# Kernel tuning notes

Measured on AMD Instinct MI355X. Metric: run time of the kernel, lower is better.

Reference implementation:

```python
import jax, jax.numpy as jnp
import numpy as np

B, NJ, NM = 64, 30, 20
N = NJ * NM          # 600 operation nodes per FJSP instance
IN_DIM, H = 2, 128


def _bn(h):
    # torch BatchNorm1d in training mode, gamma=1/beta=0 (module init), stats over all nodes
    m = h.mean(axis=(0, 1))
    v = h.var(axis=(0, 1))
    return (h - m) / jnp.sqrt(v + 1e-5)


def setup_inputs() -> dict:
    key = jax.random.key(0)
    ks = jax.random.split(key, 20)
    x = jax.random.normal(ks[0], (B, N, IN_DIM), jnp.float32)
    graph_pool = jnp.full((B, N), 1.0 / N, jnp.float32)   # average graph pooling weights
    padded_nei = jnp.zeros((1,), jnp.int32)               # unused (sum pooling path)
    adj = (jax.random.uniform(ks[1], (B, N, N)) < 0.01).astype(jnp.float32)
    adj = jnp.minimum(adj + jnp.eye(N, dtype=jnp.float32)[None], 1.0)  # self-loops
    candidate = jax.random.randint(ks[2], (B, NJ), 0, N)
    a_index = jax.random.randint(ks[3], (B,), 0, NJ)
    mask = jax.random.uniform(ks[4], (B, NJ)) < 0.2
    mask = mask.at[jnp.arange(B), a_index].set(False)     # chosen action never masked
    mask_mch = jax.random.uniform(ks[5], (B, N, NM)) < 0.3
    dur = jax.random.uniform(ks[6], (B, N, NM), dtype=jnp.float32)
    old_action = jax.random.randint(ks[7], (B,), 0, N)
    mch_pool = jax.random.normal(ks[8], (B, H), jnp.float32)

    def w(k, i, o):
        return jax.random.normal(k, (i, o), jnp.float32) * (1.0 / np.sqrt(i))

    z = lambda n: jnp.zeros((n,), jnp.float32)            # biases init to 0 in module
    return dict(
        x=x, graph_pool=graph_pool, padded_nei=padded_nei, adj=adj,
        candidate=candidate, mask=mask, mask_mch=mask_mch, dur=dur,
        a_index=a_index, old_action=old_action, mch_pool=mch_pool,
        W1_0=w(ks[9], IN_DIM, H), b1_0=z(H), W2_0=w(ks[10], H, H), b2_0=z(H),
        W1_1=w(ks[11], H, H), b1_1=z(H), W2_1=w(ks[12], H, H), b2_1=z(H),
        Wa1=w(ks[13], 3 * H, H), ba1=z(H), Wa2=w(ks[14], H, H), ba2=z(H),
        Wa3=w(ks[15], H, 1), ba3=z(1),
        Wc1=w(ks[16], H, H), bc1=z(H), Wc2=w(ks[17], H, 1), bc2=z(1),
    )


def reference(x, graph_pool, padded_nei, adj, candidate, mask, mask_mch, dur,
              a_index, old_action, mch_pool,
              W1_0, b1_0, W2_0, b2_0, W1_1, b1_1, W2_1, b2_1,
              Wa1, ba1, Wa2, ba2, Wa3, ba3, Wc1, bc1, Wc2, bc2):
    # --- GIN encoder: num_layers-1 = 2 message-passing layers, sum pooling ---
    h = x
    for (W1, b1, W2, b2) in ((W1_0, b1_0, W2_0, b2_0), (W1_1, b1_1, W2_1, b2_1)):
        pooled = jnp.einsum('bnm,bmd->bnd', adj, h)         # neighbor sum (adj has self-loops)
        h1 = jax.nn.relu(_bn(pooled @ W1 + b1))             # MLP hidden (BN inside MLP)
        h = jax.nn.relu(_bn(h1 @ W2 + b2))                  # layer BN + relu
    h_nodes = h                                             # [B, N, H]
    h_pooled = jnp.einsum('bn,bnd->bd', graph_pool, h_nodes)  # [B, H]

    # --- gather candidate features, concat pooled contexts ---
    cand_feat = jnp.take_along_axis(h_nodes, candidate[:, :, None], axis=1)  # [B, NJ, H]
    concat = jnp.concatenate([
        cand_feat,
        jnp.broadcast_to(h_pooled[:, None, :], cand_feat.shape),
        jnp.broadcast_to(mch_pool[:, None, :], cand_feat.shape)], axis=-1)   # [B, NJ, 3H]

    # --- MLPActor(3 layers, tanh) ---
    a = jnp.tanh(concat @ Wa1 + ba1)
    a = jnp.tanh(a @ Wa2 + ba2)
    scores = (a @ Wa3 + ba3).squeeze(-1) * 10.0             # [B, NJ]
    scores = jnp.where(mask, -jnp.inf, scores)
    logpi = jax.nn.log_softmax(scores, axis=1)
    pi = jnp.exp(logpi)
    log_a = jnp.take_along_axis(logpi, a_index[:, None], axis=1)[:, 0]
    entropy = -jnp.sum(jnp.where(pi > 0, pi * logpi, 0.0), axis=1)

    # --- gather action-dependent tensors (detached in torch) ---
    b_idx = jnp.arange(B)
    action_node = dur[b_idx, old_action]                    # [B, NM]
    action_feature = h_nodes[b_idx, old_action]             # [B, H]
    mask_mch_action = mask_mch[b_idx, old_action][:, None, :]  # [B, 1, NM]

    # --- MLPCritic(2 layers, tanh) ---
    v = jnp.tanh(h_pooled @ Wc1 + bc1) @ Wc2 + bc2          # [B, 1]

    sg = jax.lax.stop_gradient
    return (entropy, v, log_a, sg(action_node), sg(action_feature),
            mask_mch_action, sg(h_pooled))
```

## Files before the change

kernel.cpp:

```cpp
#include <hip/hip_runtime.h>
#include <hip/hip_bf16.h>

#define BB 64
#define NJ 30
#define NM 20
#define NN 600
#define HH 128
#define NROWS (BB*NN)
#define CAP 48

typedef __attribute__((ext_vector_type(8))) short short8;
typedef __attribute__((ext_vector_type(4))) float f32x4;

#define STATS_B   0
#define HPOOL_B   4096
#define FLAGS_B   36864
#define ZERO_B    36880
#define WTB_B     37120
#define SCORES_B  135424
#define NBRCNT_B  143104
#define NBRIDX_B  296704
#define POOLED0_B 7669504
#define T1_B      7976704
#define P1_B      27637504

#define OUT_ENT   0
#define OUT_V     64
#define OUT_LOGA  128
#define OUT_ANODE 192
#define OUT_AFEAT 1472
#define OUT_MMCH  9664
#define OUT_HPOOL 10944

__device__ __forceinline__ bool mask_at(const void* p, int layout, long i) {
    if (layout == 2) return ((const float*)p)[i] != 0.f;
    if (layout == 1) return ((const unsigned char*)p)[i] != 0;
    return ((const int*)p)[i] != 0;
}

__device__ __forceinline__ short bf16rne(float f) {
    unsigned u = __float_as_uint(f);
    return (short)((u + 0x7fffu + ((u >> 16) & 1u)) >> 16);
}
__device__ __forceinline__ float bf2f(unsigned h) {
    return __uint_as_float(h << 16);
}
__device__ __forceinline__ unsigned packbf(float a, float b) {
    return ((unsigned)(unsigned short)bf16rne(a)) |
           (((unsigned)(unsigned short)bf16rne(b)) << 16);
}

__global__ __launch_bounds__(256) void k_pre(const void* mask_p, const void* maskmch_p,
                                             int* flags,
                                             const float* __restrict__ Wa,
                                             const float* __restrict__ Wb,
                                             const float* __restrict__ Wc,
                                             unsigned short* __restrict__ wT) {
    int bid = blockIdx.x;
    int tid = threadIdx.x;
    if (bid >= 97) {
        int bid2 = bid - 97;
        int mat = bid2 >> 6;
        int idx = ((bid2 & 63) << 8) + tid;
        const float* W = mat == 0 ? Wa : (mat == 1 ? Wb : Wc);
        int k = idx >> 7, c = idx & 127;
        wT[mat * 16384 + c * HH + k] = (unsigned short)bf16rne(W[idx]);
        return;
    }
    unsigned agg = 0;
    int which;
    if (bid == 0) {
        which = 0;
        const unsigned* p = (const unsigned*)mask_p;
        unsigned w0 = (tid < 480) ? p[tid] : 0u;
        unsigned w1 = (tid + 256 < 480) ? p[tid + 256] : 0u;
        agg = w0 | w1;
    } else {
        which = 1;
        const unsigned* p = (const unsigned*)maskmch_p + (size_t)(bid - 1) * 200;
        agg = (tid < 200) ? p[tid] : 0u;
    }
    int f = 0;
    if (((agg >> 24) & 0xffu) == 0x3fu) f |= 1;
    if ((((agg >> 8) & 0xffu) == 1u) || (((agg >> 16) & 0xffu) == 1u) ||
        (((agg >> 24) & 0xffu) == 1u)) f |= 2;
#pragma unroll
    for (int off = 1; off < 64; off <<= 1) f |= __shfl_xor(f, off);
    if ((tid & 63) == 0 && f) atomicOr(&flags[which], f);
}

__global__ __launch_bounds__(256) void k_sparse(const float* __restrict__ adj,
                                                const float* __restrict__ x,
                                                int* __restrict__ nbr_cnt,
                                                int* __restrict__ nbr_idx,
                                                float* __restrict__ pooled0) {
    int wrow = blockIdx.x * 4 + (threadIdx.x >> 6);
    int lane = threadIdx.x & 63;
    int b = wrow / NN;
    const float4* arow = (const float4*)(adj + (size_t)wrow * NN);
    int* irow = nbr_idx + (size_t)wrow * CAP;
    const float* xb = x + (size_t)b * NN * 2;
    float4 vv[3];
    vv[0] = arow[lane];
    vv[1] = arow[64 + lane];
    vv[2] = (128 + lane < 150) ? arow[128 + lane] : make_float4(0.f, 0.f, 0.f, 0.f);
    int cnt = 0;
    float p0 = 0.f, p1 = 0.f;
#pragma unroll
    for (int it = 0; it < 3; ++it) {
        float4 v = vv[it];
        int col0 = it * 256 + lane * 4;
        bool m0 = v.x != 0.f, m1 = v.y != 0.f, m2 = v.z != 0.f, m3 = v.w != 0.f;
        int c_lane = (int)m0 + (int)m1 + (int)m2 + (int)m3;
        int inc = c_lane;
#pragma unroll
        for (int off = 1; off < 64; off <<= 1) {
            int t = __shfl_up(inc, off);
            if (lane >= off) inc += t;
        }
        int pos = cnt + inc - c_lane;
        if (m0) {
            if (pos < CAP) irow[pos] = col0;
            float2 xv = *(const float2*)&xb[col0 * 2];
            p0 += xv.x; p1 += xv.y; ++pos;
        }
        if (m1) {
            if (pos < CAP) irow[pos] = col0 + 1;
            float2 xv = *(const float2*)&xb[(col0 + 1) * 2];
            p0 += xv.x; p1 += xv.y; ++pos;
        }
        if (m2) {
            if (pos < CAP) irow[pos] = col0 + 2;
            float2 xv = *(const float2*)&xb[(col0 + 2) * 2];
            p0 += xv.x; p1 += xv.y; ++pos;
        }
        if (m3) {
            if (pos < CAP) irow[pos] = col0 + 3;
            float2 xv = *(const float2*)&xb[(col0 + 3) * 2];
            p0 += xv.x; p1 += xv.y; ++pos;
        }
        cnt += __shfl(inc, 63);
    }
#pragma unroll
    for (int off = 1; off < 64; off <<= 1) {
        p0 += __shfl_xor(p0, off);
        p1 += __shfl_xor(p1, off);
    }
    if (lane == 0) {
        nbr_cnt[wrow] = cnt < CAP ? cnt : CAP;
        pooled0[(size_t)wrow * 2]     = p0;
        pooled0[(size_t)wrow * 2 + 1] = p1;
    }
}

__global__ __launch_bounds__(256) void k_p0stats(const float* __restrict__ pooled0,
                                                 float* __restrict__ out5) {
    __shared__ float red[4][5];
    int i = blockIdx.x * 256 + threadIdx.x;
    float p0 = pooled0[(size_t)i * 2], p1 = pooled0[(size_t)i * 2 + 1];
    float v[5] = {p0, p1, p0 * p0, p1 * p1, p0 * p1};
#pragma unroll
    for (int j = 0; j < 5; ++j)
#pragma unroll
        for (int off = 1; off < 64; off <<= 1) v[j] += __shfl_xor(v[j], off);
    int lane = threadIdx.x & 63, w = threadIdx.x >> 6;
    if (lane == 0)
#pragma unroll
        for (int j = 0; j < 5; ++j) red[w][j] = v[j];
    __syncthreads();
    if (threadIdx.x == 0)
#pragma unroll
        for (int j = 0; j < 5; ++j)
            atomicAdd(&out5[j], red[0][j] + red[1][j] + red[2][j] + red[3][j]);
}

template<int MODE>
__global__ __launch_bounds__(256) void k_stage(const void* __restrict__ t_in_v,
                                               const float* __restrict__ pooled0,
                                               const float* __restrict__ W1,
                                               const unsigned short* __restrict__ wT,
                                               const float* __restrict__ stats_in,
                                               unsigned short* __restrict__ t_out,
                                               float* __restrict__ stats_out) {
    __shared__ float sm_mean[HH], sm_inv[HH];
    __shared__ float smS[4][32], smQ[4][32];
    int tid = threadIdx.x;
    if (MODE == 0 && tid < HH) {
        float S0 = stats_in[0], S1 = stats_in[1], Q0 = stats_in[2], Q1 = stats_in[3], P01 = stats_in[4];
        float w0 = W1[tid], w1 = W1[HH + tid];
        float m = (S0 * w0 + S1 * w1) * (1.f / NROWS);
        float eq = (Q0 * w0 * w0 + Q1 * w1 * w1 + 2.f * P01 * w0 * w1) * (1.f / NROWS);
        sm_mean[tid] = m;
        sm_inv[tid] = 1.f / sqrtf(eq - m * m + 1e-5f);
    }
    if (MODE == 1 && tid < HH) {
        float s = stats_in[tid], q = stats_in[HH + tid];
        float m = s * (1.f / NROWS);
        sm_mean[tid] = m;
        sm_inv[tid] = 1.f / sqrtf(q * (1.f / NROWS) - m * m + 1e-5f);
    }
    if (MODE != 2) __syncthreads();

    const unsigned short* tin = (const unsigned short*)t_in_v;
    int lane = tid & 63, wave = tid >> 6;
    int r16 = lane & 15, kg = lane >> 4;
    int rowbase = (blockIdx.x >> 2) * 64 + wave * 16;
    int colq = blockIdx.x & 3;

    f32x4 acc[2];
#pragma unroll
    for (int t = 0; t < 2; ++t)
#pragma unroll
        for (int i = 0; i < 4; ++i) acc[t][i] = 0.f;

    float p0 = 0.f, p1 = 0.f;
    if (MODE == 0) {
        p0 = pooled0[(size_t)(rowbase + r16) * 2];
        p1 = pooled0[(size_t)(rowbase + r16) * 2 + 1];
    }

#pragma unroll
    for (int ks = 0; ks < 4; ++ks) {
        int kb = ks * 32 + kg * 8;
        short8 afr;
        if (MODE == 2) {
            afr = *(const short8*)&tin[(size_t)(rowbase + r16) * HH + kb];
        } else {
            float av[8];
            if (MODE == 0) {
                float4 wa0 = *(const float4*)&W1[kb];
                float4 wa1 = *(const float4*)&W1[kb + 4];
                float4 wb0 = *(const float4*)&W1[HH + kb];
                float4 wb1 = *(const float4*)&W1[HH + kb + 4];
                av[0] = p0 * wa0.x + p1 * wb0.x; av[1] = p0 * wa0.y + p1 * wb0.y;
                av[2] = p0 * wa0.z + p1 * wb0.z; av[3] = p0 * wa0.w + p1 * wb0.w;
                av[4] = p0 * wa1.x + p1 * wb1.x; av[5] = p0 * wa1.y + p1 * wb1.y;
                av[6] = p0 * wa1.z + p1 * wb1.z; av[7] = p0 * wa1.w + p1 * wb1.w;
            } else {
                short8 raw = *(const short8*)&tin[(size_t)(rowbase + r16) * HH + kb];
#pragma unroll
                for (int j = 0; j < 8; ++j) av[j] = bf2f((unsigned short)raw[j]);
            }
            float4 m0 = *(const float4*)&sm_mean[kb];
            float4 m1 = *(const float4*)&sm_mean[kb + 4];
            float4 i0 = *(const float4*)&sm_inv[kb];
            float4 i1 = *(const float4*)&sm_inv[kb + 4];
            av[0] = fmaxf((av[0] - m0.x) * i0.x, 0.f);
            av[1] = fmaxf((av[1] - m0.y) * i0.y, 0.f);
            av[2] = fmaxf((av[2] - m0.z) * i0.z, 0.f);
            av[3] = fmaxf((av[3] - m0.w) * i0.w, 0.f);
            av[4] = fmaxf((av[4] - m1.x) * i1.x, 0.f);
            av[5] = fmaxf((av[5] - m1.y) * i1.y, 0.f);
            av[6] = fmaxf((av[6] - m1.z) * i1.z, 0.f);
            av[7] = fmaxf((av[7] - m1.w) * i1.w, 0.f);
#pragma unroll
            for (int j = 0; j < 8; ++j) afr[j] = bf16rne(av[j]);
        }
#pragma unroll
        for (int t = 0; t < 2; ++t) {
            short8 bfr = *(const short8*)&wT[(size_t)((colq * 2 + t) * 16 + r16) * HH + kb];
            acc[t] = __builtin_amdgcn_mfma_f32_16x16x32_bf16(afr, bfr, acc[t], 0, 0, 0);
        }
    }

#pragma unroll
    for (int t = 0; t < 2; ++t) {
        int lc = t * 16 + r16;
        int col = colq * 32 + lc;
        float s = 0.f, q = 0.f;
#pragma unroll
        for (int i = 0; i < 4; ++i) {
            float v = acc[t][i];
            t_out[(size_t)(rowbase + kg * 4 + i) * HH + col] = (unsigned short)bf16rne(v);
            s += v; q += v * v;
        }
        s += __shfl_xor(s, 16); q += __shfl_xor(q, 16);
        s += __shfl_xor(s, 32); q += __shfl_xor(q, 32);
        if (kg == 0) { smS[wave][lc] = s; smQ[wave][lc] = q; }
    }
    __syncthreads();
    if (tid < 32) {
        int col = colq * 32 + tid;
        atomicAdd(&stats_out[col],      smS[0][tid] + smS[1][tid] + smS[2][tid] + smS[3][tid]);
        atomicAdd(&stats_out[HH + col], smQ[0][tid] + smQ[1][tid] + smQ[2][tid] + smQ[3][tid]);
    }
}

__global__ __launch_bounds__(256) void k_pool1(const unsigned short* __restrict__ t1,
                                               const int* __restrict__ nbr_cnt,
                                               const int* __restrict__ nbr_idx,
                                               const float* __restrict__ stats1,
                                               unsigned short* __restrict__ pooled1) {
    __shared__ float sm_mean[HH], sm_inv[HH];
    int tid = threadIdx.x;
    if (tid < HH) {
        float s = stats1[tid], q = stats1[HH + tid];
        float m = s * (1.f / NROWS);
        sm_mean[tid] = m;
        sm_inv[tid] = 1.f / sqrtf(q * (1.f / NROWS) - m * m + 1e-5f);
    }
    __syncthreads();
    int c4 = tid & 31, rl = tid >> 5;
    int row = blockIdx.x * 8 + rl;
    int b = row / NN;
    float4 mm = *(const float4*)&sm_mean[c4 * 4];
    float4 iv = *(const float4*)&sm_inv[c4 * 4];
    int cnt = nbr_cnt[row];
    const int* ir = nbr_idx + (size_t)row * CAP;
    const unsigned short* tb = t1 + (size_t)b * NN * HH;
    float a0 = 0.f, a1 = 0.f, a2 = 0.f, a3 = 0.f;
    int i = 0;
    for (; i + 1 < cnt; i += 2) {
        int m0 = ir[i], m1 = ir[i + 1];
        uint2 w0 = *(const uint2*)&tb[(size_t)m0 * HH + c4 * 4];
        uint2 w1 = *(const uint2*)&tb[(size_t)m1 * HH + c4 * 4];
        a0 += fmaxf((bf2f(w0.x & 0xffffu) - mm.x) * iv.x, 0.f)
            + fmaxf((bf2f(w1.x & 0xffffu) - mm.x) * iv.x, 0.f);
        a1 += fmaxf((bf2f(w0.x >> 16)     - mm.y) * iv.y, 0.f)
            + fmaxf((bf2f(w1.x >> 16)     - mm.y) * iv.y, 0.f);
        a2 += fmaxf((bf2f(w0.y & 0xffffu) - mm.z) * iv.z, 0.f)
            + fmaxf((bf2f(w1.y & 0xffffu) - mm.z) * iv.z, 0.f);
        a3 += fmaxf((bf2f(w0.y >> 16)     - mm.w) * iv.w, 0.f)
            + fmaxf((bf2f(w1.y >> 16)     - mm.w) * iv.w, 0.f);
    }
    if (i < cnt) {
        int m0 = ir[i];
        uint2 w0 = *(const uint2*)&tb[(size_t)m0 * HH + c4 * 4];
        a0 += fmaxf((bf2f(w0.x & 0xffffu) - mm.x) * iv.x, 0.f);
        a1 += fmaxf((bf2f(w0.x >> 16)     - mm.y) * iv.y, 0.f);
        a2 += fmaxf((bf2f(w0.y & 0xffffu) - mm.z) * iv.z, 0.f);
        a3 += fmaxf((bf2f(w0.y >> 16)     - mm.w) * iv.w, 0.f);
    }
    uint2 o;
    o.x = packbf(a0, a1);
    o.y = packbf(a2, a3);
    *(uint2*)&pooled1[(size_t)row * HH + c4 * 4] = o;
}

__global__ __launch_bounds__(256) void k_hpool(const unsigned short* __restrict__ t3,
                                               const float* __restrict__ gp,
                                               const float* __restrict__ stats3,
                                               float* __restrict__ hpool) {
    __shared__ float sm_mean[HH], sm_inv[HH];
    __shared__ float red[8][HH];
    int tid = threadIdx.x;
    if (tid < HH) {
        float s = stats3[tid], q = stats3[HH + tid];
        float m = s * (1.f / NROWS);
        sm_mean[tid] = m;
        sm_inv[tid] = 1.f / sqrtf(q * (1.f / NROWS) - m * m + 1e-5f);
    }
    __syncthreads();
    int b = blockIdx.x >> 3, chunk = blockIdx.x & 7;
    int c4 = tid & 31, rl = tid >> 5;
    float4 mm = *(const float4*)&sm_mean[c4 * 4];
    float4 iv = *(const float4*)&sm_inv[c4 * 4];
    float a0 = 0.f, a1 = 0.f, a2 = 0.f, a3 = 0.f;
    int nend = chunk * 75 + 75;
    for (int n = chunk * 75 + rl; n < nend; n += 8) {
        float w = gp[b * NN + n];
        uint2 t = *(const uint2*)&t3[((size_t)b * NN + n) * HH + c4 * 4];
        a0 += w * fmaxf((bf2f(t.x & 0xffffu) - mm.x) * iv.x, 0.f);
        a1 += w * fmaxf((bf2f(t.x >> 16)     - mm.y) * iv.y, 0.f);
        a2 += w * fmaxf((bf2f(t.y & 0xffffu) - mm.z) * iv.z, 0.f);
        a3 += w * fmaxf((bf2f(t.y >> 16)     - mm.w) * iv.w, 0.f);
    }
    *(float4*)&red[rl][c4 * 4] = make_float4(a0, a1, a2, a3);
    __syncthreads();
    if (tid < HH) {
        float s = 0.f;
#pragma unroll
        for (int g = 0; g < 8; ++g) s += red[g][tid];
        atomicAdd(&hpool[b * HH + tid], s);
    }
}

__global__ __launch_bounds__(256) void k_actor(const unsigned short* __restrict__ t3,
                                               const int* __restrict__ cand,
                                               const float* __restrict__ hpool,
                                               const float* __restrict__ mch,
                                               const float* __restrict__ stats3,
                                               const float* __restrict__ Wa1,
                                               const float* __restrict__ ba1,
                                               const float* __restrict__ Wa2,
                                               const float* __restrict__ ba2,
                                               const float* __restrict__ Wa3,
                                               const float* __restrict__ ba3,
                                               float* __restrict__ scores) {
    __shared__ float sh_c[8 * 384];
    __shared__ float sh_a1[8 * HH];
    __shared__ float sred[8][HH];
    int tid = threadIdx.x;
    int rbase = blockIdx.x * 8;
    int c = tid & 127, slot = tid >> 7;

    float mean_c, inv_c;
    {
        float s = stats3[c], q = stats3[HH + c];
        float m = s * (1.f / NROWS);
        mean_c = m;
        inv_c = 1.f / sqrtf(q * (1.f / NROWS) - m * m + 1e-5f);
    }
#pragma unroll
    for (int rr = 0; rr < 4; ++rr) {
        int r = slot * 4 + rr;
        int row = rbase + r;
        int b = row / NJ;
        int cd = cand[row];
        float v = bf2f(t3[((size_t)b * NN + cd) * HH + c]);
        sh_c[r * 384 + c]       = fmaxf((v - mean_c) * inv_c, 0.f);
        sh_c[r * 384 + 128 + c] = hpool[b * HH + c];
        sh_c[r * 384 + 256 + c] = mch[b * HH + c];
    }
    __syncthreads();

    float acc[4] = {0.f, 0.f, 0.f, 0.f};
    for (int k = 0; k < 384; ++k) {
        float w = Wa1[(size_t)k * HH + c];
#pragma unroll
        for (int rr = 0; rr < 4; ++rr)
            acc[rr] += sh_c[(slot * 4 + rr) * 384 + k] * w;
    }
    float bb = ba1[c];
#pragma unroll
    for (int rr = 0; rr < 4; ++rr)
        sh_a1[(slot * 4 + rr) * HH + c] = tanhf(acc[rr] + bb);
    __syncthreads();

    float acc2[4] = {0.f, 0.f, 0.f, 0.f};
    for (int k = 0; k < HH; ++k) {
        float w = Wa2[(size_t)k * HH + c];
#pragma unroll
        for (int rr = 0; rr < 4; ++rr)
            acc2[rr] += sh_a1[(slot * 4 + rr) * HH + k] * w;
    }
    float w3 = Wa3[c], bb2 = ba2[c];
#pragma unroll
    for (int rr = 0; rr < 4; ++rr)
        sred[slot * 4 + rr][c] = tanhf(acc2[rr] + bb2) * w3;
    __syncthreads();
    int r = tid >> 5, l32 = tid & 31;
    float v = sred[r][l32] + sred[r][l32 + 32] + sred[r][l32 + 64] + sred[r][l32 + 96];
    v += __shfl_xor(v, 1); v += __shfl_xor(v, 2); v += __shfl_xor(v, 4);
    v += __shfl_xor(v, 8); v += __shfl_xor(v, 16);
    if (l32 == 0) scores[rbase + r] = 10.f * (v + ba3[0]);
}

__global__ __launch_bounds__(128) void k_final(const unsigned short* __restrict__ t3,
                                               const float* __restrict__ stats3,
                                               const float* __restrict__ hpool,
                                               const float* __restrict__ scores,
                                               const void* __restrict__ mask_p,
                                               const void* __restrict__ maskmch_p,
                                               const int* __restrict__ flags,
                                               const float* __restrict__ dur,
                                               const int* __restrict__ a_index,
                                               const int* __restrict__ old_action,
                                               const float* __restrict__ Wc1,
                                               const float* __restrict__ bc1,
                                               const float* __restrict__ Wc2,
                                               const float* __restrict__ bc2,
                                               float* __restrict__ out) {
    __shared__ float sm_mean[HH], sm_inv[HH], sh_hp[HH], sh_red[HH];
    __shared__ float sh_s[32], sh_lp[32];
    __shared__ int sh_m[32];
    int b = blockIdx.x, t = threadIdx.x;
    {
        float s = stats3[t], q = stats3[HH + t];
        float m = s * (1.f / NROWS);
        sm_mean[t] = m;
        sm_inv[t] = 1.f / sqrtf(q * (1.f / NROWS) - m * m + 1e-5f);
    }
    sh_hp[t] = hpool[b * HH + t];
    __syncthreads();

    float acc = bc1[t];
    for (int k = 0; k < HH; ++k) acc += sh_hp[k] * Wc1[k * HH + t];
    sh_red[t] = tanhf(acc) * Wc2[t];
    __syncthreads();
    for (int st = 64; st > 0; st >>= 1) {
        if (t < st) sh_red[t] += sh_red[t + st];
        __syncthreads();
    }
    if (t == 0) out[OUT_V + b] = sh_red[0] + bc2[0];

    int fA = flags[0], fB = flags[1];
    int layA = (fA & 1) ? 2 : ((fA & 2) ? 1 : 0);
    int layB = (fB & 1) ? 2 : ((fB & 2) ? 1 : 0);
    if (t < NJ) {
        sh_s[t] = scores[b * NJ + t];
        sh_m[t] = mask_at(mask_p, layA, (long)b * NJ + t) ? 1 : 0;
    }
    __syncthreads();
    if (t == 0) {
        float mx = -1e30f;
        for (int j = 0; j < NJ; ++j)
            if (!sh_m[j] && sh_s[j] > mx) mx = sh_s[j];
        float sum = 0.f;
        for (int j = 0; j < NJ; ++j)
            if (!sh_m[j]) sum += expf(sh_s[j] - mx);
        float lse = mx + logf(sum);
        float ent = 0.f;
        for (int j = 0; j < NJ; ++j) {
            if (!sh_m[j]) {
                float lp = sh_s[j] - lse;
                sh_lp[j] = lp;
                float pi = expf(lp);
                if (pi > 0.f) ent -= pi * lp;
            }
        }
        out[OUT_ENT + b] = ent;
        out[OUT_LOGA + b] = sh_lp[a_index[b]];
    }

    int old = old_action[b];
    if (t < NM) {
        out[OUT_ANODE + b * NM + t] = dur[((size_t)b * NN + old) * NM + t];
        out[OUT_MMCH + b * NM + t] =
            mask_at(maskmch_p, layB, ((size_t)b * NN + old) * NM + t) ? 1.f : 0.f;
    }
    {
        float v = bf2f(t3[((size_t)b * NN + old) * HH + t]);
        out[OUT_AFEAT + b * HH + t] = fmaxf((v - sm_mean[t]) * sm_inv[t], 0.f);
        out[OUT_HPOOL + b * HH + t] = sh_hp[t];
    }
}

extern "C" void kernel_launch(void* const* d_in, const int* in_sizes, int n_in,
                              void* d_out, int out_size, void* d_ws, size_t ws_size,
                              hipStream_t stream) {
    (void)in_sizes; (void)n_in; (void)out_size; (void)ws_size;
    const float* x         = (const float*)d_in[0];
    const float* gp        = (const float*)d_in[1];
    const float* adj       = (const float*)d_in[3];
    const int*   cand      = (const int*)d_in[4];
    const void*  mask_p    = d_in[5];
    const void*  maskmch_p = d_in[6];
    const float* dur       = (const float*)d_in[7];
    const int*   a_index   = (const int*)d_in[8];
    const int*   old_act   = (const int*)d_in[9];
    const float* mch_pool  = (const float*)d_in[10];
    const float* W1_0 = (const float*)d_in[11];
    const float* W2_0 = (const float*)d_in[13];
    const float* W1_1 = (const float*)d_in[15];
    const float* W2_1 = (const float*)d_in[17];
    const float* Wa1  = (const float*)d_in[19];
    const float* ba1  = (const float*)d_in[20];
    const float* Wa2  = (const float*)d_in[21];
    const float* ba2  = (const float*)d_in[22];
    const float* Wa3  = (const float*)d_in[23];
    const float* ba3  = (const float*)d_in[24];
    const float* Wc1  = (const float*)d_in[25];
    const float* bc1  = (const float*)d_in[26];
    const float* Wc2  = (const float*)d_in[27];
    const float* bc2  = (const float*)d_in[28];

    char* ws = (char*)d_ws;
    float* stats   = (float*)(ws + STATS_B);
    float* hpool   = (float*)(ws + HPOOL_B);
    int*   flags   = (int*)(ws + FLAGS_B);
    unsigned short* wtb = (unsigned short*)(ws + WTB_B);
    float* scores  = (float*)(ws + SCORES_B);
    int*   nbr_cnt = (int*)(ws + NBRCNT_B);
    int*   nbr_idx = (int*)(ws + NBRIDX_B);
    float* pooled0 = (float*)(ws + POOLED0_B);
    unsigned short* t1_16 = (unsigned short*)(ws + T1_B);
    unsigned short* p1_16 = (unsigned short*)(ws + P1_B);
    float* out     = (float*)d_out;

    hipMemsetAsync(ws, 0, ZERO_B, stream);
    k_pre<<<289, 256, 0, stream>>>(mask_p, maskmch_p, flags, W2_0, W1_1, W2_1, wtb);
    k_sparse<<<NROWS / 4, 256, 0, stream>>>(adj, x, nbr_cnt, nbr_idx, pooled0);
    k_p0stats<<<NROWS / 256, 256, 0, stream>>>(pooled0, stats);
    k_stage<0><<<2400, 256, 0, stream>>>(nullptr, pooled0, W1_0, wtb, stats, t1_16, stats + 256);
    k_pool1<<<NROWS / 8, 256, 0, stream>>>(t1_16, nbr_cnt, nbr_idx, stats + 256, p1_16);
    k_stage<2><<<2400, 256, 0, stream>>>(p1_16, nullptr, nullptr, wtb + 16384, stats, t1_16, stats + 512);
    k_stage<1><<<2400, 256, 0, stream>>>(t1_16, nullptr, nullptr, wtb + 32768, stats + 512, p1_16, stats + 768);
    k_hpool<<<BB * 8, 256, 0, stream>>>(p1_16, gp, stats + 768, hpool);
    k_actor<<<240, 256, 0, stream>>>(p1_16, cand, hpool, mch_pool, stats + 768,
                                     Wa1, ba1, Wa2, ba2, Wa3, ba3, scores);
    k_final<<<BB, 128, 0, stream>>>(p1_16, stats + 768, hpool, scores, mask_p, maskmch_p, flags,
                                    dur, a_index, old_act, Wc1, bc1, Wc2, bc2, out);
}
```

Measured before the change: 352.1 us.

## Fuse preprocessing into sparse pass, pooling into GEMM stage, and tail kernels

Folds the mask-flag and weight-transpose work into the sparse adjacency kernel. Fuses the layer-1 neighbour pooling with the following MFMA GEMM through shared memory, so the pooled intermediate is never written to global memory. Merges graph pooling, the actor MLP, the critic and the final softmax into one per-batch kernel, with the hpool/mch part of the first actor layer computed once per batch. This cuts the launch count from ten to six and removes several global round trips, but the tail now runs on only 64 blocks, and the pooling GEMM reads weights from global memory per block.

After: 395.7 us. 12.4% more time.

```diff
diff --git a/kernel.cpp b/kernel.cpp
--- a/kernel.cpp
+++ b/kernel.cpp
@@ -13,11 +13,9 @@
 typedef __attribute__((ext_vector_type(4))) float f32x4;
 
 #define STATS_B   0
-#define HPOOL_B   4096
 #define FLAGS_B   36864
 #define ZERO_B    36880
 #define WTB_B     37120
-#define SCORES_B  135424
 #define NBRCNT_B  143104
 #define NBRIDX_B  296704
 #define POOLED0_B 7669504
@@ -50,52 +48,53 @@
            (((unsigned)(unsigned short)bf16rne(b)) << 16);
 }
 
-__global__ __launch_bounds__(256) void k_pre(const void* mask_p, const void* maskmch_p,
-                                             int* flags,
-                                             const float* __restrict__ Wa,
-                                             const float* __restrict__ Wb,
-                                             const float* __restrict__ Wc,
-                                             unsigned short* __restrict__ wT) {
-    int bid = blockIdx.x;
-    int tid = threadIdx.x;
-    if (bid >= 97) {
-        int bid2 = bid - 97;
-        int mat = bid2 >> 6;
-        int idx = ((bid2 & 63) << 8) + tid;
-        const float* W = mat == 0 ? Wa : (mat == 1 ? Wb : Wc);
-        int k = idx >> 7, c = idx & 127;
-        wT[mat * 16384 + c * HH + k] = (unsigned short)bf16rne(W[idx]);
-        return;
-    }
-    unsigned agg = 0;
-    int which;
-    if (bid == 0) {
-        which = 0;
-        const unsigned* p = (const unsigned*)mask_p;
-        unsigned w0 = (tid < 480) ? p[tid] : 0u;
-        unsigned w1 = (tid + 256 < 480) ? p[tid + 256] : 0u;
-        agg = w0 | w1;
-    } else {
-        which = 1;
-        const unsigned* p = (const unsigned*)maskmch_p + (size_t)(bid - 1) * 200;
-        agg = (tid < 200) ? p[tid] : 0u;
-    }
-    int f = 0;
-    if (((agg >> 24) & 0xffu) == 0x3fu) f |= 1;
-    if ((((agg >> 8) & 0xffu) == 1u) || (((agg >> 16) & 0xffu) == 1u) ||
-        (((agg >> 24) & 0xffu) == 1u)) f |= 2;
-#pragma unroll
-    for (int off = 1; off < 64; off <<= 1) f |= __shfl_xor(f, off);
-    if ((tid & 63) == 0 && f) atomicOr(&flags[which], f);
-}
-
 __global__ __launch_bounds__(256) void k_sparse(const float* __restrict__ adj,
                                                 const float* __restrict__ x,
                                                 int* __restrict__ nbr_cnt,
                                                 int* __restrict__ nbr_idx,
-                                                float* __restrict__ pooled0) {
-    int wrow = blockIdx.x * 4 + (threadIdx.x >> 6);
-    int lane = threadIdx.x & 63;
+                                                float* __restrict__ pooled0,
+                                                const void* mask_p, const void* maskmch_p,
+                                                int* flags,
+                                                const float* __restrict__ Wa,
+                                                const float* __restrict__ Wb,
+                                                const float* __restrict__ Wc,
+                                                unsigned short* __restrict__ wT) {
+    int bid = blockIdx.x;
+    int tid = threadIdx.x;
+    if (bid < 289) {
+        if (bid >= 97) {
+            int bid2 = bid - 97;
+            int mat = bid2 >> 6;
+            int idx = ((bid2 & 63) << 8) + tid;
+            const float* W = mat == 0 ? Wa : (mat == 1 ? Wb : Wc);
+            int k = idx >> 7, c = idx & 127;
+            wT[mat * 16384 + c * HH + k] = (unsigned short)bf16rne(W[idx]);
+        } else {
+            unsigned agg = 0;
+            int which;
+            if (bid == 0) {
+                which = 0;
+                const unsigned* p = (const unsigned*)mask_p;
+                unsigned w0 = (tid < 480) ? p[tid] : 0u;
+                unsigned w1 = (tid + 256 < 480) ? p[tid + 256] : 0u;
+                agg = w0 | w1;
+            } else {
+                which = 1;
+                const unsigned* p = (const unsigned*)maskmch_p + (size_t)(bid - 1) * 200;
+                agg = (tid < 200) ? p[tid] : 0u;
+            }
+            int f = 0;
+            if (((agg >> 24) & 0xffu) == 0x3fu) f |= 1;
+            if ((((agg >> 8) & 0xffu) == 1u) || (((agg >> 16) & 0xffu) == 1u) ||
+                (((agg >> 24) & 0xffu) == 1u)) f |= 2;
+#pragma unroll
+            for (int off = 1; off < 64; off <<= 1) f |= __shfl_xor(f, off);
+            if ((tid & 63) == 0 && f) atomicOr(&flags[which], f);
+        }
+    }
+
+    int wrow = bid * 4 + (tid >> 6);
+    int lane = tid & 63;
     int b = wrow / NN;
     const float4* arow = (const float4*)(adj + (size_t)wrow * NN);
     int* irow = nbr_idx + (size_t)wrow * CAP;
@@ -199,7 +198,7 @@
         sm_mean[tid] = m;
         sm_inv[tid] = 1.f / sqrtf(q * (1.f / NROWS) - m * m + 1e-5f);
     }
-    if (MODE != 2) __syncthreads();
+    __syncthreads();
 
     const unsigned short* tin = (const unsigned short*)t_in_v;
     int lane = tid & 63, wave = tid >> 6;
@@ -223,9 +222,7 @@
     for (int ks = 0; ks < 4; ++ks) {
         int kb = ks * 32 + kg * 8;
         short8 afr;
-        if (MODE == 2) {
-            afr = *(const short8*)&tin[(size_t)(rowbase + r16) * HH + kb];
-        } else {
+        {
             float av[8];
             if (MODE == 0) {
                 float4 wa0 = *(const float4*)&W1[kb];
@@ -286,12 +283,16 @@
     }
 }
 
-__global__ __launch_bounds__(256) void k_pool1(const unsigned short* __restrict__ t1,
-                                               const int* __restrict__ nbr_cnt,
-                                               const int* __restrict__ nbr_idx,
-                                               const float* __restrict__ stats1,
-                                               unsigned short* __restrict__ pooled1) {
+__global__ __launch_bounds__(256) void k_poolstage(const unsigned short* __restrict__ t1,
+                                                   const int* __restrict__ nbr_cnt,
+                                                   const int* __restrict__ nbr_idx,
+                                                   const float* __restrict__ stats1,
+                                                   const unsigned short* __restrict__ wT,
+                                                   unsigned short* __restrict__ t_out,
+                                                   float* __restrict__ stats_out) {
     __shared__ float sm_mean[HH], sm_inv[HH];
+    __shared__ unsigned short shA[32 * HH];
+    __shared__ float smS[4][HH], smQ[4][HH];
     int tid = threadIdx.x;
     if (tid < HH) {
         float s = stats1[tid], q = stats1[HH + tid];
@@ -300,199 +301,214 @@
         sm_inv[tid] = 1.f / sqrtf(q * (1.f / NROWS) - m * m + 1e-5f);
     }
     __syncthreads();
-    int c4 = tid & 31, rl = tid >> 5;
-    int row = blockIdx.x * 8 + rl;
-    int b = row / NN;
-    float4 mm = *(const float4*)&sm_mean[c4 * 4];
-    float4 iv = *(const float4*)&sm_inv[c4 * 4];
-    int cnt = nbr_cnt[row];
-    const int* ir = nbr_idx + (size_t)row * CAP;
-    const unsigned short* tb = t1 + (size_t)b * NN * HH;
-    float a0 = 0.f, a1 = 0.f, a2 = 0.f, a3 = 0.f;
-    int i = 0;
-    for (; i + 1 < cnt; i += 2) {
-        int m0 = ir[i], m1 = ir[i + 1];
-        uint2 w0 = *(const uint2*)&tb[(size_t)m0 * HH + c4 * 4];
-        uint2 w1 = *(const uint2*)&tb[(size_t)m1 * HH + c4 * 4];
-        a0 += fmaxf((bf2f(w0.x & 0xffffu) - mm.x) * iv.x, 0.f)
-            + fmaxf((bf2f(w1.x & 0xffffu) - mm.x) * iv.x, 0.f);
-        a1 += fmaxf((bf2f(w0.x >> 16)     - mm.y) * iv.y, 0.f)
-            + fmaxf((bf2f(w1.x >> 16)     - mm.y) * iv.y, 0.f);
-        a2 += fmaxf((bf2f(w0.y & 0xffffu) - mm.z) * iv.z, 0.f)
-            + fmaxf((bf2f(w1.y & 0xffffu) - mm.z) * iv.z, 0.f);
-        a3 += fmaxf((bf2f(w0.y >> 16)     - mm.w) * iv.w, 0.f)
-            + fmaxf((bf2f(w1.y >> 16)     - mm.w) * iv.w, 0.f);
-    }
-    if (i < cnt) {
-        int m0 = ir[i];
-        uint2 w0 = *(const uint2*)&tb[(size_t)m0 * HH + c4 * 4];
-        a0 += fmaxf((bf2f(w0.x & 0xffffu) - mm.x) * iv.x, 0.f);
-        a1 += fmaxf((bf2f(w0.x >> 16)     - mm.y) * iv.y, 0.f);
-        a2 += fmaxf((bf2f(w0.y & 0xffffu) - mm.z) * iv.z, 0.f);
-        a3 += fmaxf((bf2f(w0.y >> 16)     - mm.w) * iv.w, 0.f);
-    }
-    uint2 o;
-    o.x = packbf(a0, a1);
-    o.y = packbf(a2, a3);
-    *(uint2*)&pooled1[(size_t)row * HH + c4 * 4] = o;
-}
-
-__global__ __launch_bounds__(256) void k_hpool(const unsigned short* __restrict__ t3,
-                                               const float* __restrict__ gp,
-                                               const float* __restrict__ stats3,
-                                               float* __restrict__ hpool) {
-    __shared__ float sm_mean[HH], sm_inv[HH];
-    __shared__ float red[8][HH];
-    int tid = threadIdx.x;
+    int rowbase = blockIdx.x * 32;
+
+    {
+        int r = tid >> 3, cg = tid & 7;
+        int row = rowbase + r;
+        int b = row / NN;
+        int cnt = nbr_cnt[row];
+        const int* ir = nbr_idx + (size_t)row * CAP;
+        const unsigned short* tb = t1 + (size_t)b * NN * HH + cg * 16;
+        float accv[16];
+#pragma unroll
+        for (int j = 0; j < 16; ++j) accv[j] = 0.f;
+        float mloc[16], iloc[16];
+#pragma unroll
+        for (int j = 0; j < 16; ++j) {
+            mloc[j] = sm_mean[cg * 16 + j];
+            iloc[j] = sm_inv[cg * 16 + j];
+        }
+        for (int i = 0; i < cnt; ++i) {
+            int m_ = ir[i];
+            const unsigned short* p = tb + (size_t)m_ * HH;
+            uint2 w0 = *(const uint2*)(p);
+            uint2 w1 = *(const uint2*)(p + 4);
+            uint2 w2 = *(const uint2*)(p + 8);
+            uint2 w3 = *(const uint2*)(p + 12);
+            unsigned wsv[8] = {w0.x, w0.y, w1.x, w1.y, w2.x, w2.y, w3.x, w3.y};
+#pragma unroll
+            for (int j = 0; j < 8; ++j) {
+                accv[2 * j]     += fmaxf((bf2f(wsv[j] & 0xffffu) - mloc[2 * j])     * iloc[2 * j], 0.f);
+                accv[2 * j + 1] += fmaxf((bf2f(wsv[j] >> 16)     - mloc[2 * j + 1]) * iloc[2 * j + 1], 0.f);
+            }
+        }
+        unsigned short* dst = &shA[r * HH + cg * 16];
+#pragma unroll
+        for (int j = 0; j < 8; ++j)
+            *(unsigned*)(dst + 2 * j) = packbf(accv[2 * j], accv[2 * j + 1]);
+    }
+    __syncthreads();
+
+    int lane = tid & 63, w = tid >> 6;
+    int r16 = lane & 15, kg = lane >> 4;
+    int rhalf = w & 1, chalf = w >> 1;
+    int rloc = rhalf * 16 + r16;
+    short8 afr[4];
+#pragma unroll
+    for (int ks = 0; ks < 4; ++ks)
+        afr[ks] = *(const short8*)&shA[rloc * HH + ks * 32 + kg * 8];
+    f32x4 acc[4];
+#pragma unroll
+    for (int t = 0; t < 4; ++t)
+#pragma unroll
+        for (int i = 0; i < 4; ++i) acc[t][i] = 0.f;
+#pragma unroll
+    for (int t = 0; t < 4; ++t) {
+        int coltile = chalf * 4 + t;
+#pragma unroll
+        for (int ks = 0; ks < 4; ++ks) {
+            short8 bfr = *(const short8*)&wT[(size_t)(coltile * 16 + r16) * HH + ks * 32 + kg * 8];
+            acc[t] = __builtin_amdgcn_mfma_f32_16x16x32_bf16(afr[ks], bfr, acc[t], 0, 0, 0);
+        }
+    }
+#pragma unroll
+    for (int t = 0; t < 4; ++t) {
+        int col = (chalf * 4 + t) * 16 + r16;
+        float s = 0.f, q = 0.f;
+#pragma unroll
+        for (int i = 0; i < 4; ++i) {
+            float v = acc[t][i];
+            t_out[(size_t)(rowbase + rhalf * 16 + kg * 4 + i) * HH + col] = (unsigned short)bf16rne(v);
+            s += v; q += v * v;
+        }
+        s += __shfl_xor(s, 16); q += __shfl_xor(q, 16);
+        s += __shfl_xor(s, 32); q += __shfl_xor(q, 32);
+        if (kg == 0) { smS[w][col] = s; smQ[w][col] = q; }
+    }
+    __syncthreads();
+    if (tid < HH) {
+        int col = tid;
+        float s, q;
+        if (col < 64) { s = smS[0][col] + smS[1][col]; q = smQ[0][col] + smQ[1][col]; }
+        else          { s = smS[2][col] + smS[3][col]; q = smQ[2][col] + smQ[3][col]; }
+        atomicAdd(&stats_out[col], s);
+        atomicAdd(&stats_out[HH + col], q);
+    }
+}
+
+__global__ __launch_bounds__(256) void k_tail(const unsigned short* __restrict__ t3,
+                                              const float* __restrict__ gp,
+                                              const float* __restrict__ stats3,
+                                              const int* __restrict__ cand,
+                                              const float* __restrict__ mch,
+                                              const void* __restrict__ mask_p,
+                                              const void* __restrict__ maskmch_p,
+                                              const int* __restrict__ flags,
+                                              const float* __restrict__ dur,
+                                              const int* __restrict__ a_index,
+                                              const int* __restrict__ old_action,
+                                              const float* __restrict__ Wa1,
+                                              const float* __restrict__ ba1,
+                                              const float* __restrict__ Wa2,
+                                              const float* __restrict__ ba2,
+                                              const float* __restrict__ Wa3,
+                                              const float* __restrict__ ba3,
+                                              const float* __restrict__ Wc1,
+                                              const float* __restrict__ bc1,
+                                              const float* __restrict__ Wc2,
+                                              const float* __restrict__ bc2,
+                                              float* __restrict__ out) {
+    __shared__ float sm_mean[HH], sm_inv[HH], sh_hp[HH], sh_mch[HH], sh_red[HH];
+    __shared__ float red8[8][HH];
+    __shared__ float sh_cand[NJ][HH];
+    __shared__ float sh_a1[NJ][HH];
+    __shared__ float sh_sc[NJ][132];
+    __shared__ float sh_s[32], sh_lp[32];
+    __shared__ int sh_m[32];
+    int b = blockIdx.x, tid = threadIdx.x;
+
     if (tid < HH) {
         float s = stats3[tid], q = stats3[HH + tid];
         float m = s * (1.f / NROWS);
         sm_mean[tid] = m;
         sm_inv[tid] = 1.f / sqrtf(q * (1.f / NROWS) - m * m + 1e-5f);
-    }
-    __syncthreads();
-    int b = blockIdx.x >> 3, chunk = blockIdx.x & 7;
-    int c4 = tid & 31, rl = tid >> 5;
-    float4 mm = *(const float4*)&sm_mean[c4 * 4];
-    float4 iv = *(const float4*)&sm_inv[c4 * 4];
-    float a0 = 0.f, a1 = 0.f, a2 = 0.f, a3 = 0.f;
-    int nend = chunk * 75 + 75;
-    for (int n = chunk * 75 + rl; n < nend; n += 8) {
-        float w = gp[b * NN + n];
-        uint2 t = *(const uint2*)&t3[((size_t)b * NN + n) * HH + c4 * 4];
-        a0 += w * fmaxf((bf2f(t.x & 0xffffu) - mm.x) * iv.x, 0.f);
-        a1 += w * fmaxf((bf2f(t.x >> 16)     - mm.y) * iv.y, 0.f);
-        a2 += w * fmaxf((bf2f(t.y & 0xffffu) - mm.z) * iv.z, 0.f);
-        a3 += w * fmaxf((bf2f(t.y >> 16)     - mm.w) * iv.w, 0.f);
-    }
-    *(float4*)&red[rl][c4 * 4] = make_float4(a0, a1, a2, a3);
+        sh_mch[tid] = mch[b * HH + tid];
+    }
+    __syncthreads();
+
+    {
+        int c4 = tid & 31, rl = tid >> 5;
+        float4 mm = *(const float4*)&sm_mean[c4 * 4];
+        float4 iv = *(const float4*)&sm_inv[c4 * 4];
+        float a0 = 0.f, a1 = 0.f, a2 = 0.f, a3 = 0.f;
+        for (int n = rl; n < NN; n += 8) {
+            float w = gp[b * NN + n];
+            uint2 t = *(const uint2*)&t3[((size_t)b * NN + n) * HH + c4 * 4];
+            a0 += w * fmaxf((bf2f(t.x & 0xffffu) - mm.x) * iv.x, 0.f);
+            a1 += w * fmaxf((bf2f(t.x >> 16)     - mm.y) * iv.y, 0.f);
+            a2 += w * fmaxf((bf2f(t.y & 0xffffu) - mm.z) * iv.z, 0.f);
+            a3 += w * fmaxf((bf2f(t.y >> 16)     - mm.w) * iv.w, 0.f);
+        }
+        *(float4*)&red8[rl][c4 * 4] = make_float4(a0, a1, a2, a3);
+    }
     __syncthreads();
     if (tid < HH) {
         float s = 0.f;
 #pragma unroll
-        for (int g = 0; g < 8; ++g) s += red[g][tid];
-        atomicAdd(&hpool[b * HH + tid], s);
-    }
-}
-
-__global__ __launch_bounds__(256) void k_actor(const unsigned short* __restrict__ t3,
-                                               const int* __restrict__ cand,
-                                               const float* __restrict__ hpool,
-                                               const float* __restrict__ mch,
-                                               const float* __restrict__ stats3,
-                                               const float* __restrict__ Wa1,
-                                               const float* __restrict__ ba1,
-                                               const float* __restrict__ Wa2,
-                                               const float* __restrict__ ba2,
-                                               const float* __restrict__ Wa3,
-                                               const float* __restrict__ ba3,
-                                               float* __restrict__ scores) {
-    __shared__ float sh_c[8 * 384];
-    __shared__ float sh_a1[8 * HH];
-    __shared__ float sred[8][HH];
-    int tid = threadIdx.x;
-    int rbase = blockIdx.x * 8;
+        for (int g = 0; g < 8; ++g) s += red8[g][tid];
+        sh_hp[tid] = s;
+    }
+    __syncthreads();
+
     int c = tid & 127, slot = tid >> 7;
-
-    float mean_c, inv_c;
+    float mean_c = sm_mean[c], inv_c = sm_inv[c];
+
+    for (int r = slot; r < NJ; r += 2) {
+        int cd = cand[b * NJ + r];
+        float v = bf2f(t3[((size_t)b * NN + cd) * HH + c]);
+        sh_cand[r][c] = fmaxf((v - mean_c) * inv_c, 0.f);
+    }
     {
-        float s = stats3[c], q = stats3[HH + c];
-        float m = s * (1.f / NROWS);
-        mean_c = m;
-        inv_c = 1.f / sqrtf(q * (1.f / NROWS) - m * m + 1e-5f);
-    }
-#pragma unroll
-    for (int rr = 0; rr < 4; ++rr) {
-        int r = slot * 4 + rr;
-        int row = rbase + r;
-        int b = row / NJ;
-        int cd = cand[row];
-        float v = bf2f(t3[((size_t)b * NN + cd) * HH + c]);
-        sh_c[r * 384 + c]       = fmaxf((v - mean_c) * inv_c, 0.f);
-        sh_c[r * 384 + 128 + c] = hpool[b * HH + c];
-        sh_c[r * 384 + 256 + c] = mch[b * HH + c];
-    }
-    __syncthreads();
-
-    float acc[4] = {0.f, 0.f, 0.f, 0.f};
-    for (int k = 0; k < 384; ++k) {
-        float w = Wa1[(size_t)k * HH + c];
-#pragma unroll
-        for (int rr = 0; rr < 4; ++rr)
-            acc[rr] += sh_c[(slot * 4 + rr) * 384 + k] * w;
-    }
-    float bb = ba1[c];
-#pragma unroll
-    for (int rr = 0; rr < 4; ++rr)
-        sh_a1[(slot * 4 + rr) * HH + c] = tanhf(acc[rr] + bb);
-    __syncthreads();
-
-    float acc2[4] = {0.f, 0.f, 0.f, 0.f};
-    for (int k = 0; k < HH; ++k) {
-        float w = Wa2[(size_t)k * HH + c];
-#pragma unroll
-        for (int rr = 0; rr < 4; ++rr)
-            acc2[rr] += sh_a1[(slot * 4 + rr) * HH + k] * w;
-    }
-    float w3 = Wa3[c], bb2 = ba2[c];
-#pragma unroll
-    for (int rr = 0; rr < 4; ++rr)
-        sred[slot * 4 + rr][c] = tanhf(acc2[rr] + bb2) * w3;
-    __syncthreads();
-    int r = tid >> 5, l32 = tid & 31;
-    float v = sred[r][l32] + sred[r][l32 + 32] + sred[r][l32 + 64] + sred[r][l32 + 96];
-    v += __shfl_xor(v, 1); v += __shfl_xor(v, 2); v += __shfl_xor(v, 4);
-    v += __shfl_xor(v, 8); v += __shfl_xor(v, 16);
-    if (l32 == 0) scores[rbase + r] = 10.f * (v + ba3[0]);
-}
-
-__global__ __launch_bounds__(128) void k_final(const unsigned short* __restrict__ t3,
-                                               const float* __restrict__ stats3,
-                                               const float* __restrict__ hpool,
-                                               const float* __restrict__ scores,
-                                               const void* __restrict__ mask_p,
-                                               const void* __restrict__ maskmch_p,
-                                               const int* __restrict__ flags,
-                                               const float* __restrict__ dur,
-                                               const int* __restrict__ a_index,
-                                               const int* __restrict__ old_action,
-                                               const float* __restrict__ Wc1,
-                                               const float* __restrict__ bc1,
-                                               const float* __restrict__ Wc2,
-                                               const float* __restrict__ bc2,
-                                               float* __restrict__ out) {
-    __shared__ float sm_mean[HH], sm_inv[HH], sh_hp[HH], sh_red[HH];
-    __shared__ float sh_s[32], sh_lp[32];
-    __shared__ int sh_m[32];
-    int b = blockIdx.x, t = threadIdx.x;
+        float part = 0.f;
+        const float* src = (slot == 0) ? sh_hp : sh_mch;
+        const float* Wp  = Wa1 + (size_t)(slot == 0 ? 128 : 256) * HH;
+        for (int k = 0; k < HH; ++k) part += src[k] * Wp[(size_t)k * HH + c];
+        red8[slot][c] = part;
+    }
+    __syncthreads();
+    float b2 = red8[0][c] + red8[1][c] + ba1[c];
+
+    for (int r = slot; r < NJ; r += 2) {
+        float acc = b2;
+        for (int k = 0; k < HH; ++k) acc += sh_cand[r][k] * Wa1[(size_t)k * HH + c];
+        sh_a1[r][c] = tanhf(acc);
+    }
+    __syncthreads();
+
     {
-        float s = stats3[t], q = stats3[HH + t];
-        float m = s * (1.f / NROWS);
-        sm_mean[t] = m;
-        sm_inv[t] = 1.f / sqrtf(q * (1.f / NROWS) - m * m + 1e-5f);
-    }
-    sh_hp[t] = hpool[b * HH + t];
-    __syncthreads();
-
-    float acc = bc1[t];
-    for (int k = 0; k < HH; ++k) acc += sh_hp[k] * Wc1[k * HH + t];
-    sh_red[t] = tanhf(acc) * Wc2[t];
+        float w3 = Wa3[c], bb2 = ba2[c];
+        for (int r = slot; r < NJ; r += 2) {
+            float acc2 = bb2;
+            for (int k = 0; k < HH; ++k) acc2 += sh_a1[r][k] * Wa2[(size_t)k * HH + c];
+            sh_sc[r][c] = tanhf(acc2) * w3;
+        }
+    }
+    __syncthreads();
+    if (tid < NJ) {
+        float s = 0.f;
+        for (int c2 = 0; c2 < HH; ++c2) s += sh_sc[tid][c2];
+        sh_s[tid] = 10.f * (s + ba3[0]);
+    }
+
+    if (tid < HH) {
+        float a = bc1[tid];
+        for (int k = 0; k < HH; ++k) a += sh_hp[k] * Wc1[(size_t)k * HH + tid];
+        sh_red[tid] = tanhf(a) * Wc2[tid];
+    }
     __syncthreads();
     for (int st = 64; st > 0; st >>= 1) {
-        if (t < st) sh_red[t] += sh_red[t + st];
+        if (tid < st) sh_red[tid] += sh_red[tid + st];
         __syncthreads();
     }
-    if (t == 0) out[OUT_V + b] = sh_red[0] + bc2[0];
+    if (tid == 0) out[OUT_V + b] = sh_red[0] + bc2[0];
 
     int fA = flags[0], fB = flags[1];
     int layA = (fA & 1) ? 2 : ((fA & 2) ? 1 : 0);
     int layB = (fB & 1) ? 2 : ((fB & 2) ? 1 : 0);
-    if (t < NJ) {
-        sh_s[t] = scores[b * NJ + t];
-        sh_m[t] = mask_at(mask_p, layA, (long)b * NJ + t) ? 1 : 0;
-    }
-    __syncthreads();
-    if (t == 0) {
+    if (tid < NJ) sh_m[tid] = mask_at(mask_p, layA, (long)b * NJ + tid) ? 1 : 0;
+    __syncthreads();
+    if (tid == 0) {
         float mx = -1e30f;
         for (int j = 0; j < NJ; ++j)
             if (!sh_m[j] && sh_s[j] > mx) mx = sh_s[j];
@@ -514,15 +530,15 @@
     }
 
     int old = old_action[b];
-    if (t < NM) {
-        out[OUT_ANODE + b * NM + t] = dur[((size_t)b * NN + old) * NM + t];
-        out[OUT_MMCH + b * NM + t] =
-            mask_at(maskmch_p, layB, ((size_t)b * NN + old) * NM + t) ? 1.f : 0.f;
-    }
-    {
-        float v = bf2f(t3[((size_t)b * NN + old) * HH + t]);
-        out[OUT_AFEAT + b * HH + t] = fmaxf((v - sm_mean[t]) * sm_inv[t], 0.f);
-        out[OUT_HPOOL + b * HH + t] = sh_hp[t];
+    if (tid < NM) {
+        out[OUT_ANODE + b * NM + tid] = dur[((size_t)b * NN + old) * NM + tid];
+        out[OUT_MMCH + b * NM + tid] =
+            mask_at(maskmch_p, layB, ((size_t)b * NN + old) * NM + tid) ? 1.f : 0.f;
+    }
+    if (tid < HH) {
+        float v = bf2f(t3[((size_t)b * NN + old) * HH + tid]);
+        out[OUT_AFEAT + b * HH + tid] = fmaxf((v - mean_c) * inv_c, 0.f);
+        out[OUT_HPOOL + b * HH + tid] = sh_hp[tid];
     }
 }
 
@@ -557,28 +573,25 @@
 
     char* ws = (char*)d_ws;
     float* stats   = (float*)(ws + STATS_B);
-    float* hpool   = (float*)(ws + HPOOL_B);
     int*   flags   = (int*)(ws + FLAGS_B);
     unsigned short* wtb = (unsigned short*)(ws + WTB_B);
-    float* scores  = (float*)(ws + SCORES_B);
     int*   nbr_cnt = (int*)(ws + NBRCNT_B);
     int*   nbr_idx = (int*)(ws + NBRIDX_B);
     float* pooled0 = (float*)(ws + POOLED0_B);
     unsigned short* t1_16 = (unsigned short*)(ws + T1_B);
-    unsigned short* p1_16 = (unsigned short*)(ws + P1_B);
+    unsigned short* t2_16 = (unsigned short*)(ws + P1_B);
     float* out     = (float*)d_out;
 
     hipMemsetAsync(ws, 0, ZERO_B, stream);
-    k_pre<<<289, 256, 0, stream>>>(mask_p, maskmch_p, flags, W2_0, W1_1, W2_1, wtb);
-    k_sparse<<<NROWS / 4, 256, 0, stream>>>(adj, x, nbr_cnt, nbr_idx, pooled0);
+    k_sparse<<<NROWS / 4, 256, 0, stream>>>(adj, x, nbr_cnt, nbr_idx, pooled0,
+                                            mask_p, maskmch_p, flags, W2_0, W1_1, W2_1, wtb);
     k_p0stats<<<NROWS / 256, 256, 0, stream>>>(pooled0, stats);
     k_stage<0><<<2400, 256, 0, stream>>>(nullptr, pooled0, W1_0, wtb, stats, t1_16, stats + 256);
-    k_pool1<<<NROWS / 8, 256, 0, stream>>>(t1_16, nbr_cnt, nbr_idx, stats + 256, p1_16);
-    k_stage<2><<<2400, 256, 0, stream>>>(p1_16, nullptr, nullptr, wtb + 16384, stats, t1_16, stats + 512);
-    k_stage<1><<<2400, 256, 0, stream>>>(t1_16, nullptr, nullptr, wtb + 32768, stats + 512, p1_16, stats + 768);
-    k_hpool<<<BB * 8, 256, 0, stream>>>(p1_16, gp, stats + 768, hpool);
-    k_actor<<<240, 256, 0, stream>>>(p1_16, cand, hpool, mch_pool, stats + 768,
-                                     Wa1, ba1, Wa2, ba2, Wa3, ba3, scores);
-    k_final<<<BB, 128, 0, stream>>>(p1_16, stats + 768, hpool, scores, mask_p, maskmch_p, flags,
-                                    dur, a_index, old_act, Wc1, bc1, Wc2, bc2, out);
-}
+    k_poolstage<<<NROWS / 32, 256, 0, stream>>>(t1_16, nbr_cnt, nbr_idx, stats + 256,
+                                                wtb + 16384, t2_16, stats + 512);
+    k_stage<1><<<2400, 256, 0, stream>>>(t2_16, nullptr, nullptr, wtb + 32768, stats + 512,
+                                         t1_16, stats + 768);
+    k_tail<<<BB, 256, 0, stream>>>(t1_16, gp, stats + 768, cand, mch_pool,
+                                   mask_p, maskmch_p, flags, dur, a_index, old_act,
+                                   Wa1, ba1, Wa2, ba2, Wa3, ba3, Wc1, bc1, Wc2, bc2, out);
+}
```
